# Kernel optimization log

Hardware: AMD Instinct MI355X
Metric: run time of the kernel (lower is better)

The kernel has to match this reference:

```python
import jax, jax.numpy as jnp
import numpy as np

B, N, D, H = 4, 2048, 1024, 16
DH = D // H  # 64
EPS = 1e-5


def setup_inputs() -> dict:
    key = jax.random.key(0)
    k1, k2, k3, k4 = jax.random.split(key, 4)
    return {
        "x": jax.random.normal(k1, (B, N, D), dtype=jnp.float32),
        "g_ln": jnp.ones((D,), dtype=jnp.float32),
        "Wq": jax.random.normal(k2, (D, D), dtype=jnp.float32) * 0.02,
        "Wkv": jax.random.normal(k3, (D, 2 * D), dtype=jnp.float32) * 0.02,
        "Wo": jax.random.normal(k4, (D, D), dtype=jnp.float32) * 0.02,
    }


def reference(x, g_ln, Wq, Wkv, Wo):
    # LayerNorm (gamma only, no bias), as in repo-style LayerNorm
    mu = jnp.mean(x, axis=-1, keepdims=True)
    var = jnp.mean(jnp.square(x - mu), axis=-1, keepdims=True)
    xn = (x - mu) * jax.lax.rsqrt(var + EPS) * g_ln

    b, n, d = xn.shape
    q = (xn @ Wq).reshape(b, n, H, DH).transpose(0, 2, 1, 3)  # b h n d
    kv = xn @ Wkv
    k, v = jnp.split(kv, 2, axis=-1)
    k = k.reshape(b, n, H, DH).transpose(0, 2, 1, 3)
    v = v.reshape(b, n, H, DH).transpose(0, 2, 1, 3)

    scale = DH ** -0.5
    dots = jnp.einsum('bhid,bhjd->bhij', q, k) * scale

    # causal mask: mask out j > i
    mask_value = -jnp.finfo(dots.dtype).max
    causal = jnp.triu(jnp.ones((n, n), dtype=bool), k=1)
    dots = jnp.where(causal, mask_value, dots)

    # softmax in float32 (attn_fn = partial(F.softmax, dtype=torch.float32))
    attn = jax.nn.softmax(dots.astype(jnp.float32), axis=-1).astype(dots.dtype)

    out = jnp.einsum('bhij,bhjd->bhid', attn, v)
    out = out.transpose(0, 2, 1, 3).reshape(b, n, d)  # b n (h d)
    return out @ Wo
```

## Files before the change

### kernel.cpp

```cpp
#include <hip/hip_runtime.h>

typedef __bf16 bf16x8 __attribute__((ext_vector_type(8)));
typedef float  f32x4  __attribute__((ext_vector_type(4)));
typedef unsigned short u16;

typedef __attribute__((address_space(3))) unsigned lds_u32;
typedef __attribute__((address_space(1))) unsigned glob_u32;

__device__ __forceinline__ void gll16(const void* g, void* l) {
  __builtin_amdgcn_global_load_lds(
      (const glob_u32*)(unsigned long long)g,
      (lds_u32*)(unsigned)(unsigned long long)l, 16, 0, 0);
}

__device__ __forceinline__ u16 cvt_bf16(float f) {
  union { float f; unsigned u; } c; c.f = f;
  unsigned u = c.u;
  return (u16)((u + 0x7FFFu + ((u >> 16) & 1u)) >> 16);
}

#define QSCALE 0.18033688011112042f

__global__ void __launch_bounds__(256) transpose_cvt(const float* __restrict__ W,
                                                     u16* __restrict__ WT,
                                                     int K, int N) {
  __shared__ float t[32][33];
  int n0 = blockIdx.x * 32, k0 = blockIdx.y * 32;
  int tx = threadIdx.x, ty = threadIdx.y;
#pragma unroll
  for (int i = 0; i < 4; i++)
    t[ty + i * 8][tx] = W[(size_t)(k0 + ty + i * 8) * N + n0 + tx];
  __syncthreads();
#pragma unroll
  for (int i = 0; i < 4; i++)
    WT[(size_t)(n0 + ty + i * 8) * K + k0 + tx] = cvt_bf16(t[tx][ty + i * 8]);
}

__global__ void __launch_bounds__(256) ln_kernel(const float* __restrict__ x,
                                                 const float* __restrict__ g,
                                                 u16* __restrict__ xn) {
  int row = blockIdx.x, tid = threadIdx.x;
  const float4* xr = (const float4*)(x + (size_t)row * 1024);
  float4 v = xr[tid];
  float s  = v.x + v.y + v.z + v.w;
  float ss = v.x * v.x + v.y * v.y + v.z * v.z + v.w * v.w;
#pragma unroll
  for (int off = 32; off > 0; off >>= 1) {
    s  += __shfl_down(s, off);
    ss += __shfl_down(ss, off);
  }
  __shared__ float red[8];
  if ((tid & 63) == 0) { red[(tid >> 6) * 2] = s; red[(tid >> 6) * 2 + 1] = ss; }
  __syncthreads();
  s  = red[0] + red[2] + red[4] + red[6];
  ss = red[1] + red[3] + red[5] + red[7];
  float mean = s * (1.0f / 1024.0f);
  float var  = ss * (1.0f / 1024.0f) - mean * mean;
  float inv  = rsqrtf(var + 1e-5f);
  float4 gv = ((const float4*)g)[tid];
  unsigned p0 = (unsigned)cvt_bf16((v.x - mean) * inv * gv.x) |
                ((unsigned)cvt_bf16((v.y - mean) * inv * gv.y) << 16);
  unsigned p1 = (unsigned)cvt_bf16((v.z - mean) * inv * gv.z) |
                ((unsigned)cvt_bf16((v.w - mean) * inv * gv.w) << 16);
  uint2 o; o.x = p0; o.y = p1;
  *(uint2*)(xn + (size_t)row * 1024 + tid * 4) = o;
}

template <int EPI>
__global__ void __launch_bounds__(256) gemm_bt(const u16* __restrict__ A,
                                               const u16* __restrict__ BT,
                                               u16* __restrict__ oQ, u16* __restrict__ oK,
                                               u16* __restrict__ oVt, float* __restrict__ oF,
                                               int M, int N, int K) {
  __shared__ u16 smem[128 * 128];
  u16* As = smem;
  u16* Bs = smem + 128 * 64;
  int tiles_n = N >> 7;
  int cpx = gridDim.x >> 3;
  int wg  = (int)blockIdx.x;
  int swz = (wg & 7) * cpx + (wg >> 3);
  int tm = swz / tiles_n, tn = swz % tiles_n;
  int tid = threadIdx.x, w = tid >> 6, l = tid & 63;
  int wr = w >> 1, wc = w & 1;
  f32x4 acc[4][4] = {};
  const u16* Abase = A + (size_t)(tm * 128) * K;
  const u16* Bbase = BT + (size_t)(tn * 128) * K;

  for (int k0 = 0; k0 < K; k0 += 64) {
#pragma unroll
    for (int t = 0; t < 4; t++) {
      int gi  = t * 256 + tid;
      int o   = gi * 16;
      int row = o >> 7;
      int sb  = o ^ ((row & 7) << 4);
      int col = (sb >> 1) & 63;
      gll16(Abase + (size_t)row * K + k0 + col, (char*)As + t * 4096 + w * 1024);
      gll16(Bbase + (size_t)row * K + k0 + col, (char*)Bs + t * 4096 + w * 1024);
    }
    __syncthreads();
#pragma unroll
    for (int ks = 0; ks < 2; ks++) {
      bf16x8 af[4], bfr[4];
      int kb = ks * 64 + ((l >> 4) << 4);
#pragma unroll
      for (int m = 0; m < 4; m++) {
        int row  = wr * 64 + m * 16 + (l & 15);
        int byte = (row * 128 + kb) ^ ((l & 7) << 4);
        af[m] = *(const bf16x8*)((const char*)As + byte);
      }
#pragma unroll
      for (int n = 0; n < 4; n++) {
        int row  = wc * 64 + n * 16 + (l & 15);
        int byte = (row * 128 + kb) ^ ((l & 7) << 4);
        bfr[n] = *(const bf16x8*)((const char*)Bs + byte);
      }
#pragma unroll
      for (int m = 0; m < 4; m++)
#pragma unroll
        for (int n = 0; n < 4; n++)
          acc[m][n] = __builtin_amdgcn_mfma_f32_16x16x32_bf16(af[m], bfr[n], acc[m][n], 0, 0, 0);
    }
    __syncthreads();
  }

  if constexpr (EPI == 0) {
    int c_base = tn * 128;
    bool isV = (c_base >= 2048);
    float qs = (c_base < 1024) ? QSCALE : 1.0f;
#pragma unroll
    for (int m = 0; m < 4; m++)
#pragma unroll
      for (int n = 0; n < 4; n++)
#pragma unroll
        for (int r = 0; r < 4; r++) {
          int rt2 = wr * 64 + m * 16 + ((l >> 4) << 2) + r;
          int c2  = wc * 64 + n * 16 + (l & 15);
          u16 bv16 = cvt_bf16(acc[m][n][r] * qs);
          int byte = isV ? ((c2 * 256 + rt2 * 2) ^ ((c2 & 7) << 4))
                         : ((rt2 * 256 + c2 * 2) ^ ((rt2 & 7) << 4));
          *(u16*)((char*)smem + byte) = bv16;
        }
    __syncthreads();
    int b = (tm * 128) >> 11;
    int nbase = (tm * 128) & 2047;
#pragma unroll
    for (int i = 0; i < 8; i++) {
      int ch = i * 256 + tid;
      int row = ch >> 4, off = ch & 15;
      uint4 d = *(const uint4*)((const char*)smem + ((row * 256 + off * 16) ^ ((row & 7) << 4)));
      if (isV) {
        int dh = row & 63;
        int h  = ((c_base - 2048) >> 6) + (row >> 6);
        *(uint4*)(oVt + ((((size_t)b * 16 + h) * 64) + dh) * 2048 + nbase + off * 8) = d;
      } else {
        int cg = c_base + off * 8;
        int nn = nbase + row;
        if (cg < 1024) {
          int h = cg >> 6, dh0 = cg & 63;
          *(uint4*)(oQ + ((((size_t)b * 16 + h) * 2048) + nn) * 64 + dh0) = d;
        } else {
          int c2g = cg - 1024, h = c2g >> 6, dh0 = c2g & 63;
          *(uint4*)(oK + ((((size_t)b * 16 + h) * 2048) + nn) * 64 + dh0) = d;
        }
      }
    }
  } else {
#pragma unroll
    for (int m = 0; m < 4; m++)
#pragma unroll
      for (int n = 0; n < 4; n++)
#pragma unroll
        for (int r = 0; r < 4; r++) {
          int rt = tm * 128 + wr * 64 + m * 16 + ((l >> 4) << 2) + r;
          int c  = tn * 128 + wc * 64 + n * 16 + (l & 15);
          oF[(size_t)rt * 1024 + c] = acc[m][n][r];
        }
  }
}

__global__ void __launch_bounds__(64, 2) attn_kernel(const u16* __restrict__ Q,
                                                     const u16* __restrict__ Kb,
                                                     const u16* __restrict__ Vt,
                                                     u16* __restrict__ Ao) {
  __shared__ u16 P[32 * 64];
  int bx = blockIdx.x;
  int bh = ((bx & 7) << 3) | (bx >> 8);
  int pair = (bx >> 3) & 31;
  int l = threadIdx.x;
  const u16* Qb    = Q  + (size_t)bh * 2048 * 64;
  const u16* Kbase = Kb + (size_t)bh * 2048 * 64;
  const u16* Vbase = Vt + (size_t)bh * 64 * 2048;
  char* Pw = (char*)P;
  int b = bh >> 4, h = bh & 15;

#pragma unroll
  for (int seg = 0; seg < 2; seg++) {
    int ws = seg ? (63 - pair) : pair;
    int q0 = ws * 32;
    int nkb = (ws >> 1) + 1;

    bf16x8 aq[2][2];
#pragma unroll
    for (int m = 0; m < 2; m++)
#pragma unroll
      for (int ks = 0; ks < 2; ks++)
        aq[m][ks] = *(const bf16x8*)(Qb + (size_t)(q0 + m * 16 + (l & 15)) * 64 + ks * 32 + ((l >> 4) << 3));

    f32x4 O[2][4] = {};
    float mrun[2][4], lpart[2][4];
#pragma unroll
    for (int m = 0; m < 2; m++)
#pragma unroll
      for (int r = 0; r < 4; r++) { mrun[m][r] = -1e30f; lpart[m][r] = 0.f; }

    bf16x8 bk[4][2], bkn[4][2];
#pragma unroll
    for (int nf = 0; nf < 4; nf++)
#pragma unroll
      for (int ks = 0; ks < 2; ks++)
        bk[nf][ks] = *(const bf16x8*)(Kbase + (size_t)(nf * 16 + (l & 15)) * 64 + ks * 32 + ((l >> 4) << 3));

    for (int kbi = 0; kbi < nkb; kbi++) {
      int k0 = kbi * 64;
      bf16x8 bv[4][2];
#pragma unroll
      for (int nf = 0; nf < 4; nf++)
#pragma unroll
        for (int ks = 0; ks < 2; ks++)
          bv[nf][ks] = *(const bf16x8*)(Vbase + (size_t)(nf * 16 + (l & 15)) * 2048 + k0 + ks * 32 + ((l >> 4) << 3));
      if (kbi + 1 < nkb) {
        int k1 = k0 + 64;
#pragma unroll
        for (int nf = 0; nf < 4; nf++)
#pragma unroll
          for (int ks = 0; ks < 2; ks++)
            bkn[nf][ks] = *(const bf16x8*)(Kbase + (size_t)(k1 + nf * 16 + (l & 15)) * 64 + ks * 32 + ((l >> 4) << 3));
      }

      f32x4 s[2][4] = {};
#pragma unroll
      for (int m = 0; m < 2; m++)
#pragma unroll
        for (int nf = 0; nf < 4; nf++)
#pragma unroll
          for (int ks = 0; ks < 2; ks++)
            s[m][nf] = __builtin_amdgcn_mfma_f32_16x16x32_bf16(aq[m][ks], bk[nf][ks], s[m][nf], 0, 0, 0);

      if (kbi == nkb - 1) {
        int colb = k0 + (l & 15);
#pragma unroll
        for (int m = 0; m < 2; m++) {
          int rowb = q0 + m * 16 + ((l >> 4) << 2);
#pragma unroll
          for (int nf = 0; nf < 4; nf++) {
            int col = colb + nf * 16;
#pragma unroll
            for (int r = 0; r < 4; r++)
              if (col > rowb + r) s[m][nf][r] = -1e30f;
          }
        }
      }

      float lmx[2][4];
      bool need = false;
#pragma unroll
      for (int m = 0; m < 2; m++)
#pragma unroll
        for (int r = 0; r < 4; r++) {
          lmx[m][r] = fmaxf(fmaxf(s[m][0][r], s[m][1][r]), fmaxf(s[m][2][r], s[m][3][r]));
          need |= (lmx[m][r] > mrun[m][r] + 8.0f);
        }
      if (__any(need)) {
#pragma unroll
        for (int m = 0; m < 2; m++)
#pragma unroll
          for (int r = 0; r < 4; r++) {
            float mx = lmx[m][r];
            mx = fmaxf(mx, __shfl_xor(mx, 1));
            mx = fmaxf(mx, __shfl_xor(mx, 2));
            mx = fmaxf(mx, __shfl_xor(mx, 4));
            mx = fmaxf(mx, __shfl_xor(mx, 8));
            float mn = fmaxf(mrun[m][r], mx);
            float sc = __builtin_amdgcn_exp2f(mrun[m][r] - mn);
            mrun[m][r] = mn;
            lpart[m][r] *= sc;
#pragma unroll
            for (int nf = 0; nf < 4; nf++) O[m][nf][r] *= sc;
          }
      }

#pragma unroll
      for (int m = 0; m < 2; m++)
#pragma unroll
        for (int r = 0; r < 4; r++) {
          int rowl = m * 16 + ((l >> 4) << 2) + r;
          float ps = 0.f;
#pragma unroll
          for (int nf = 0; nf < 4; nf++) {
            float p = __builtin_amdgcn_exp2f(s[m][nf][r] - mrun[m][r]);
            ps += p;
            int byte = (rowl * 128 + ((nf * 16 + (l & 15)) << 1)) ^ ((rowl & 7) << 4);
            *(u16*)(Pw + byte) = cvt_bf16(p);
          }
          lpart[m][r] += ps;
        }

      bf16x8 pa[2][2];
#pragma unroll
      for (int m = 0; m < 2; m++)
#pragma unroll
        for (int ks = 0; ks < 2; ks++) {
          int row  = m * 16 + (l & 15);
          int byte = (row * 128 + ks * 64 + ((l >> 4) << 4)) ^ ((row & 7) << 4);
          pa[m][ks] = *(const bf16x8*)(Pw + byte);
        }
#pragma unroll
      for (int m = 0; m < 2; m++)
#pragma unroll
        for (int nf = 0; nf < 4; nf++)
#pragma unroll
          for (int ks = 0; ks < 2; ks++)
            O[m][nf] = __builtin_amdgcn_mfma_f32_16x16x32_bf16(pa[m][ks], bv[nf][ks], O[m][nf], 0, 0, 0);

#pragma unroll
      for (int nf = 0; nf < 4; nf++)
#pragma unroll
        for (int ks = 0; ks < 2; ks++) bk[nf][ks] = bkn[nf][ks];
    }

#pragma unroll
    for (int m = 0; m < 2; m++)
#pragma unroll
      for (int r = 0; r < 4; r++) {
        float ls = lpart[m][r];
        ls += __shfl_xor(ls, 1);
        ls += __shfl_xor(ls, 2);
        ls += __shfl_xor(ls, 4);
        ls += __shfl_xor(ls, 8);
        float rinv = 1.0f / ls;
        int row = q0 + m * 16 + ((l >> 4) << 2) + r;
#pragma unroll
        for (int nf = 0; nf < 4; nf++) {
          int col = h * 64 + nf * 16 + (l & 15);
          Ao[((size_t)b * 2048 + row) * 1024 + col] = cvt_bf16(O[m][nf][r] * rinv);
        }
      }
  }
}

extern "C" void kernel_launch(void* const* d_in, const int* in_sizes, int n_in,
                              void* d_out, int out_size, void* d_ws, size_t ws_size,
                              hipStream_t stream) {
  const float* x   = (const float*)d_in[0];
  const float* g   = (const float*)d_in[1];
  const float* Wq  = (const float*)d_in[2];
  const float* Wkv = (const float*)d_in[3];
  const float* Wo  = (const float*)d_in[4];
  float* out = (float*)d_out;
  char* ws = (char*)d_ws;

  u16* WT  = (u16*)(ws);
  u16* WoT = (u16*)(ws + 6291456);
  u16* xn  = (u16*)(ws + 8388608);
  u16* Qb  = (u16*)(ws + 25165824);
  u16* Kb  = (u16*)(ws + 41943040);
  u16* Vt  = (u16*)(ws + 58720256);
  u16* Ao  = (u16*)(ws + 75497472);

  transpose_cvt<<<dim3(32, 32), dim3(32, 8), 0, stream>>>(Wq, WT, 1024, 1024);
  transpose_cvt<<<dim3(64, 32), dim3(32, 8), 0, stream>>>(Wkv, WT + 1024 * 1024, 1024, 2048);
  transpose_cvt<<<dim3(32, 32), dim3(32, 8), 0, stream>>>(Wo, WoT, 1024, 1024);
  ln_kernel<<<8192, 256, 0, stream>>>(x, g, xn);
  gemm_bt<0><<<64 * 24, 256, 0, stream>>>(xn, WT, Qb, Kb, Vt, nullptr, 8192, 3072, 1024);
  attn_kernel<<<2048, 64, 0, stream>>>(Qb, Kb, Vt, Ao);
  gemm_bt<1><<<64 * 8, 256, 0, stream>>>(Ao, WoT, nullptr, nullptr, nullptr, out, 8192, 1024, 1024);
}
```

Measured before the change: 318.5 us.

## Split attention key loop across two waves and merge partial softmax via LDS

Each attention block now runs two wavefronts. They take alternating 64-key blocks of the causal range, and each keeps its own running max, sum and O accumulator. After the loop, wave 1 writes its O tile and row statistics to shared memory, and wave 0 rescales and combines both partials before writing bf16 output. The goal is to halve the serial key-loop length per query tile and raise the number of active waves. The cost is extra LDS traffic, three block barriers per segment, and wave 1 sitting idle during the final merge.

```diff
diff --git a/kernel.cpp b/kernel.cpp
--- a/kernel.cpp
+++ b/kernel.cpp
@@ -178,19 +178,20 @@
   }
 }
 
-__global__ void __launch_bounds__(64, 2) attn_kernel(const u16* __restrict__ Q,
-                                                     const u16* __restrict__ Kb,
-                                                     const u16* __restrict__ Vt,
-                                                     u16* __restrict__ Ao) {
-  __shared__ u16 P[32 * 64];
+__global__ void __launch_bounds__(128, 2) attn_kernel(const u16* __restrict__ Q,
+                                                      const u16* __restrict__ Kb,
+                                                      const u16* __restrict__ Vt,
+                                                      u16* __restrict__ Ao) {
+  __shared__ u16 P[2][32 * 64];
+  __shared__ float ml1[64];
   int bx = blockIdx.x;
   int bh = ((bx & 7) << 3) | (bx >> 8);
   int pair = (bx >> 3) & 31;
-  int l = threadIdx.x;
+  int tid = threadIdx.x, w = tid >> 6, l = tid & 63;
   const u16* Qb    = Q  + (size_t)bh * 2048 * 64;
   const u16* Kbase = Kb + (size_t)bh * 2048 * 64;
   const u16* Vbase = Vt + (size_t)bh * 64 * 2048;
-  char* Pw = (char*)P;
+  char* Pw = (char*)&P[w][0];
   int b = bh >> 4, h = bh & 15;
 
 #pragma unroll
@@ -218,9 +219,9 @@
     for (int nf = 0; nf < 4; nf++)
 #pragma unroll
       for (int ks = 0; ks < 2; ks++)
-        bk[nf][ks] = *(const bf16x8*)(Kbase + (size_t)(nf * 16 + (l & 15)) * 64 + ks * 32 + ((l >> 4) << 3));
-
-    for (int kbi = 0; kbi < nkb; kbi++) {
+        bk[nf][ks] = *(const bf16x8*)(Kbase + (size_t)(w * 64 + nf * 16 + (l & 15)) * 64 + ks * 32 + ((l >> 4) << 3));
+
+    for (int kbi = w; kbi < nkb; kbi += 2) {
       int k0 = kbi * 64;
       bf16x8 bv[4][2];
 #pragma unroll
@@ -228,8 +229,8 @@
 #pragma unroll
         for (int ks = 0; ks < 2; ks++)
           bv[nf][ks] = *(const bf16x8*)(Vbase + (size_t)(nf * 16 + (l & 15)) * 2048 + k0 + ks * 32 + ((l >> 4) << 3));
-      if (kbi + 1 < nkb) {
-        int k1 = k0 + 64;
+      if (kbi + 2 < nkb) {
+        int k1 = k0 + 128;
 #pragma unroll
         for (int nf = 0; nf < 4; nf++)
 #pragma unroll
@@ -328,23 +329,69 @@
         for (int ks = 0; ks < 2; ks++) bk[nf][ks] = bkn[nf][ks];
     }
 
+    float lfull[2][4];
 #pragma unroll
     for (int m = 0; m < 2; m++)
 #pragma unroll
       for (int r = 0; r < 4; r++) {
-        float ls = lpart[m][r];
-        ls += __shfl_xor(ls, 1);
-        ls += __shfl_xor(ls, 2);
-        ls += __shfl_xor(ls, 4);
-        ls += __shfl_xor(ls, 8);
-        float rinv = 1.0f / ls;
-        int row = q0 + m * 16 + ((l >> 4) << 2) + r;
-#pragma unroll
-        for (int nf = 0; nf < 4; nf++) {
-          int col = h * 64 + nf * 16 + (l & 15);
-          Ao[((size_t)b * 2048 + row) * 1024 + col] = cvt_bf16(O[m][nf][r] * rinv);
-        }
-      }
+        float v = lpart[m][r];
+        v += __shfl_xor(v, 1);
+        v += __shfl_xor(v, 2);
+        v += __shfl_xor(v, 4);
+        v += __shfl_xor(v, 8);
+        lfull[m][r] = v;
+      }
+
+    __syncthreads();
+    if (w == 1) {
+      float* Ob = (float*)&P[0][0];
+#pragma unroll
+      for (int m = 0; m < 2; m++)
+#pragma unroll
+        for (int nf = 0; nf < 4; nf++)
+#pragma unroll
+          for (int r = 0; r < 4; r++) {
+            int idx = (m * 4 + nf) * 4 + r;
+            Ob[l * 32 + ((idx + l) & 31)] = O[m][nf][r];
+          }
+      if ((l & 15) == 0) {
+#pragma unroll
+        for (int m = 0; m < 2; m++)
+#pragma unroll
+          for (int r = 0; r < 4; r++) {
+            int row = m * 16 + (l >> 4) * 4 + r;
+            ml1[row * 2]     = mrun[m][r];
+            ml1[row * 2 + 1] = lfull[m][r];
+          }
+      }
+    }
+    __syncthreads();
+    if (w == 0) {
+      const float* Ob = (const float*)&P[0][0];
+#pragma unroll
+      for (int m = 0; m < 2; m++)
+#pragma unroll
+        for (int r = 0; r < 4; r++) {
+          int rowl = m * 16 + (l >> 4) * 4 + r;
+          float m1 = ml1[rowl * 2];
+          float l1 = ml1[rowl * 2 + 1];
+          float m0 = mrun[m][r];
+          float ms = fmaxf(m0, m1);
+          float a0 = __builtin_amdgcn_exp2f(m0 - ms);
+          float a1 = __builtin_amdgcn_exp2f(m1 - ms);
+          float rinv = 1.0f / (lfull[m][r] * a0 + l1 * a1);
+          int row = q0 + rowl;
+#pragma unroll
+          for (int nf = 0; nf < 4; nf++) {
+            int idx = (m * 4 + nf) * 4 + r;
+            float o1 = Ob[l * 32 + ((idx + l) & 31)];
+            float ov = (O[m][nf][r] * a0 + o1 * a1) * rinv;
+            int col = h * 64 + nf * 16 + (l & 15);
+            Ao[((size_t)b * 2048 + row) * 1024 + col] = cvt_bf16(ov);
+          }
+        }
+    }
+    __syncthreads();
   }
 }
 
@@ -372,6 +419,6 @@
   transpose_cvt<<<dim3(32, 32), dim3(32, 8), 0, stream>>>(Wo, WoT, 1024, 1024);
   ln_kernel<<<8192, 256, 0, stream>>>(x, g, xn);
   gemm_bt<0><<<64 * 24, 256, 0, stream>>>(xn, WT, Qb, Kb, Vt, nullptr, 8192, 3072, 1024);
-  attn_kernel<<<2048, 64, 0, stream>>>(Qb, Kb, Vt, Ao);
+  attn_kernel<<<2048, 128, 0, stream>>>(Qb, Kb, Vt, Ao);
   gemm_bt<1><<<64 * 8, 256, 0, stream>>>(Ao, WoT, nullptr, nullptr, nullptr, out, 8192, 1024, 1024);
 }
```

Measured after the change: 345.7 us. +8.5%, slower.
